# Performance work log

Measured on AMD Instinct MI355X. Metric: run time of the kernel, lower is better.

The kernel has to match this reference:

```python
import jax, jax.numpy as jnp
import numpy as np

B, S, D = 4, 2048, 1024
E = 8            # num_experts
F = 4096         # expert hidden dim (4*D)
T = B * S        # tokens
CAP = 1280       # capacity = ceil(1.25 * T / E)


def setup_inputs() -> dict:
    key = jax.random.key(0)
    k1, k2, k3, k4 = jax.random.split(key, 4)
    inputs = jax.random.normal(k1, (B, S, D), dtype=jnp.float32)
    gate_w = jax.random.normal(k2, (D, E), dtype=jnp.float32) / np.sqrt(D)
    w1 = jax.random.normal(k3, (E, D, F), dtype=jnp.float32) / np.sqrt(D)
    w2 = jax.random.normal(k4, (E, F, D), dtype=jnp.float32) / np.sqrt(F)
    return {"inputs": inputs, "gate_w": gate_w, "w1": w1, "w2": w2}


def reference(inputs, gate_w, w1, w2):
    tokens = inputs.reshape(-1, D)                       # [T, D]
    logits = tokens @ gate_w                             # [T, E] (gate, no bias)
    probs = jax.nn.softmax(logits, axis=-1)
    expert_idx = jnp.argmax(probs, axis=-1)              # top-1 routing
    mask1 = jax.nn.one_hot(expert_idx, E, dtype=tokens.dtype)        # [T, E]
    # position of each token within its chosen expert's queue
    pos = (jnp.cumsum(mask1, axis=0) - 1.0).astype(jnp.int32)        # [T, E]
    # one_hot of out-of-range (>= CAP) positions is all-zero -> capacity drop
    sec_mask = mask1[:, :, None] * jax.nn.one_hot(pos, CAP, dtype=tokens.dtype)  # [T, E, C]
    combine_weights = probs[:, :, None] * sec_mask       # [T, E, C]
    # dispatch: matmul(sec_mask.permute(1,2,0), tokens) -> [E, C, D]
    expert_input = jnp.einsum('tec,td->ecd', sec_mask, tokens)
    # grouped per-expert FFN
    h = jax.nn.relu(jnp.einsum('ecd,edf->ecf', expert_input, w1))    # [E, C, F]
    expert_output = jnp.einsum('ecf,efd->ecd', h, w2)                # [E, C, D]
    # combine: [T, E*C] @ [E*C, D]
    out = jnp.einsum('tec,ecd->td', combine_weights, expert_output)  # [T, D]
    return out.reshape(inputs.shape)
```

## Files before the change

kernel.cpp:

```cpp
#include <hip/hip_runtime.h>
#include <hip/hip_bf16.h>

#define TOKENS   8192
#define DDIM     1024
#define NEXP     8
#define FDIM     4096
#define CAPACITY 1280
#define NYT      10

typedef __attribute__((ext_vector_type(8))) __bf16 bf16x8;
typedef __attribute__((ext_vector_type(4))) __bf16 bf16x4;
typedef __attribute__((ext_vector_type(4))) float  f32x4;

typedef __attribute__((address_space(1))) const void gvoid_t;
typedef __attribute__((address_space(3))) void       lvoid_t;

__device__ __forceinline__ void async16(const void* g, void* l) {
  __builtin_amdgcn_global_load_lds((gvoid_t*)g, (lvoid_t*)l, 16, 0, 0);
}

__global__ void gate_kernel(const float* __restrict__ x, const float* __restrict__ gw,
                            int* __restrict__ eidx, float* __restrict__ prob) {
  const int t = blockIdx.x;
  const int lane = threadIdx.x;
  const float* xp = x + (size_t)t * DDIM;
  float acc[NEXP];
#pragma unroll
  for (int e = 0; e < NEXP; ++e) acc[e] = 0.f;
#pragma unroll 4
  for (int i = 0; i < DDIM / 64; ++i) {
    const int d = i * 64 + lane;
    const float xv = xp[d];
    const f32x4 g0 = *(const f32x4*)(gw + d * NEXP);
    const f32x4 g1 = *(const f32x4*)(gw + d * NEXP + 4);
    acc[0] += xv * g0[0]; acc[1] += xv * g0[1];
    acc[2] += xv * g0[2]; acc[3] += xv * g0[3];
    acc[4] += xv * g1[0]; acc[5] += xv * g1[1];
    acc[6] += xv * g1[2]; acc[7] += xv * g1[3];
  }
#pragma unroll
  for (int e = 0; e < NEXP; ++e) {
    float v = acc[e];
#pragma unroll
    for (int off = 32; off; off >>= 1) v += __shfl_xor(v, off);
    acc[e] = v;
  }
  if (lane == 0) {
    float m = acc[0]; int mi = 0;
#pragma unroll
    for (int e = 1; e < NEXP; ++e) if (acc[e] > m) { m = acc[e]; mi = e; }
    float s = 0.f;
#pragma unroll
    for (int e = 0; e < NEXP; ++e) s += __expf(acc[e] - m);
    eidx[t] = mi;
    prob[t] = 1.f / s;
  }
}

__global__ void scan_kernel(const int* __restrict__ eidx, int* __restrict__ src,
                            int* __restrict__ counts) {
  __shared__ int buf[2][NEXP][256];
  const int tid = threadIdx.x;
  for (int i = tid; i < NEXP * CAPACITY; i += 256) src[i] = -1;
  const int t0 = tid * (TOKENS / 256);
#pragma unroll
  for (int e = 0; e < NEXP; ++e) buf[0][e][tid] = 0;
  for (int k = 0; k < TOKENS / 256; ++k) {
    const int e = eidx[t0 + k];
    buf[0][e][tid]++;
  }
  __syncthreads();
  int cur = 0;
  for (int off = 1; off < 256; off <<= 1) {
#pragma unroll
    for (int e = 0; e < NEXP; ++e) {
      int v = buf[cur][e][tid];
      if (tid >= off) v += buf[cur][e][tid - off];
      buf[cur ^ 1][e][tid] = v;
    }
    __syncthreads();
    cur ^= 1;
  }
  if (tid < NEXP) counts[tid] = buf[cur][tid][255];
#pragma unroll
  for (int e = 0; e < NEXP; ++e)
    buf[cur ^ 1][e][tid] = (tid > 0) ? buf[cur][e][tid - 1] : 0;
  for (int k = 0; k < TOKENS / 256; ++k) {
    const int t = t0 + k;
    const int e = eidx[t];
    const int p = buf[cur ^ 1][e][tid]++;
    if (p < CAPACITY) src[e * CAPACITY + p] = t;
  }
}

__global__ void dispatch_kernel(const float* __restrict__ tokens, const int* __restrict__ src,
                                __bf16* __restrict__ Xb) {
  const int slot = blockIdx.x;
  const int tid  = threadIdx.x;
  const int t = src[slot];
  bf16x4* dst = (bf16x4*)(Xb + (size_t)slot * DDIM);
  bf16x4 o;
  if (t >= 0) {
    const f32x4 v = ((const f32x4*)(tokens + (size_t)t * DDIM))[tid];
    o[0] = (__bf16)v[0]; o[1] = (__bf16)v[1]; o[2] = (__bf16)v[2]; o[3] = (__bf16)v[3];
  } else {
    o[0] = (__bf16)0.f; o[1] = (__bf16)0.f; o[2] = (__bf16)0.f; o[3] = (__bf16)0.f;
  }
  dst[tid] = o;
}

__global__ void transpose_convert_kernel(const float* __restrict__ w, __bf16* __restrict__ wt,
                                         int R, int C) {
  __shared__ __bf16 tile[64][66];
  const int e = blockIdx.z;
  const float* wp = w + (size_t)e * R * C;
  __bf16* op = wt + (size_t)e * R * C;
  const int c0 = blockIdx.x * 64, r0 = blockIdx.y * 64;
  const int tid = threadIdx.x;
#pragma unroll
  for (int p = 0; p < 4; ++p) {
    const int r = p * 16 + (tid >> 4);
    const int c = (tid & 15) * 4;
    const f32x4 v = *(const f32x4*)(wp + (size_t)(r0 + r) * C + c0 + c);
    tile[r][c]     = (__bf16)v[0]; tile[r][c + 1] = (__bf16)v[1];
    tile[r][c + 2] = (__bf16)v[2]; tile[r][c + 3] = (__bf16)v[3];
  }
  __syncthreads();
#pragma unroll
  for (int p = 0; p < 2; ++p) {
    const int c  = p * 32 + (tid >> 3);
    const int rg = (tid & 7) * 8;
    bf16x8 o;
#pragma unroll
    for (int i = 0; i < 8; ++i) o[i] = tile[rg + i][c];
    *(bf16x8*)(op + (size_t)(c0 + c) * R + r0 + rg) = o;
  }
}

__global__ __launch_bounds__(256, 2)
void gemm1_kernel(const __bf16* __restrict__ A, const __bf16* __restrict__ B,
                  __bf16* __restrict__ Cbf, const int* __restrict__ counts,
                  int K, size_t sA, size_t sB, size_t sC) {
  constexpr int N  = FDIM;
  constexpr int NX = N / 128;
  __shared__ __bf16 lds[2][128 * 64];

  const int nwg = NX * NYT * NEXP;
  int wg = blockIdx.x;
  wg = (wg & 7) * (nwg >> 3) + (wg >> 3);
  const int e   = wg / (NX * NYT);
  const int rem = wg - e * (NX * NYT);
  const int ty  = rem % NYT;
  const int tx  = rem / NYT;
  const int m0  = ty * 128, n0 = tx * 128;

  const int cnt   = counts[e];
  const int tiles = (cnt + 127) >> 7;
  if (ty >= ((tiles < NYT) ? tiles : NYT)) return;

  const __bf16* Ae = A + (size_t)e * sA;
  const __bf16* Be = B + (size_t)e * sB;
  const int tid = threadIdx.x;
  const int wid = tid >> 6, lane = tid & 63;
  const int wm = wid >> 1, wn = wid & 1;
  const int rl = lane & 15, gl = lane >> 4;

  f32x4 acc[4][4];
#pragma unroll
  for (int m = 0; m < 4; ++m)
#pragma unroll
    for (int n = 0; n < 4; ++n) acc[m][n] = (f32x4){0.f, 0.f, 0.f, 0.f};

  for (int kt = 0; kt < K; kt += 64) {
#pragma unroll
    for (int i = 0; i < 4; ++i) {
      const int s   = (wid * 4 + i) * 64 + lane;
      const int row = s >> 3;
      const int cg  = (s & 7) ^ (row & 7);
      async16(Ae + (size_t)(m0 + row) * K + kt + cg * 8, &lds[0][(wid * 4 + i) * 512]);
      async16(Be + (size_t)(n0 + row) * K + kt + cg * 8, &lds[1][(wid * 4 + i) * 512]);
    }
    __syncthreads();
    const char* la = (const char*)&lds[0][0];
    const char* lb = (const char*)&lds[1][0];
#pragma unroll
    for (int kk = 0; kk < 2; ++kk) {
      bf16x8 af[4], bv[4];
#pragma unroll
      for (int m = 0; m < 4; ++m) {
        const int rowin = wm * 64 + m * 16 + rl;
        af[m] = *(const bf16x8*)(la + rowin * 128 + (((kk * 4 + gl) ^ (rowin & 7)) * 16));
      }
#pragma unroll
      for (int n = 0; n < 4; ++n) {
        const int rowin = wn * 64 + n * 16 + rl;
        bv[n] = *(const bf16x8*)(lb + rowin * 128 + (((kk * 4 + gl) ^ (rowin & 7)) * 16));
      }
#pragma unroll
      for (int m = 0; m < 4; ++m)
#pragma unroll
        for (int n = 0; n < 4; ++n)
          acc[m][n] = __builtin_amdgcn_mfma_f32_16x16x32_bf16(af[m], bv[n], acc[m][n], 0, 0, 0);
    }
    __syncthreads();
  }

  __bf16* Ce = Cbf + (size_t)e * sC;
#pragma unroll
  for (int m = 0; m < 4; ++m)
#pragma unroll
    for (int j = 0; j < 4; ++j) {
      const int row = m0 + wm * 64 + m * 16 + gl * 4 + j;
#pragma unroll
      for (int n = 0; n < 4; ++n) {
        const int col = n0 + wn * 64 + n * 16 + rl;
        float v = acc[m][n][j];
        v = v > 0.f ? v : 0.f;
        Ce[(size_t)row * N + col] = (__bf16)v;
      }
    }
}

__global__ __launch_bounds__(256, 2)
void gemm2_kernel(const __bf16* __restrict__ A, const float* __restrict__ Bw,
                  float* __restrict__ out, const int* __restrict__ src,
                  const float* __restrict__ prob, const int* __restrict__ counts,
                  int K, size_t sA, size_t sBw) {
  constexpr int N  = DDIM;
  constexpr int NX = N / 128;
  __shared__ __bf16 lds[2][128 * 64];

  const int nwg = NX * NYT * NEXP;
  int wg = blockIdx.x;
  wg = (wg & 7) * (nwg >> 3) + (wg >> 3);
  const int e   = wg / (NX * NYT);
  const int rem = wg - e * (NX * NYT);
  const int ty  = rem % NYT;
  const int tx  = rem / NYT;
  const int m0  = ty * 128, n0 = tx * 128;

  const int cnt   = counts[e];
  const int tiles = (cnt + 127) >> 7;
  if (ty >= ((tiles < NYT) ? tiles : NYT)) return;

  const __bf16* Ae = A + (size_t)e * sA;
  const float*  Be = Bw + (size_t)e * sBw;
  const int tid = threadIdx.x;
  const int wid = tid >> 6, lane = tid & 63;
  const int wm = wid >> 1, wn = wid & 1;
  const int rl = lane & 15, gl = lane >> 4;
  const int nq = tid & 31;
  const int kb = tid >> 5;

  f32x4 acc[4][4];
#pragma unroll
  for (int m = 0; m < 4; ++m)
#pragma unroll
    for (int n = 0; n < 4; ++n) acc[m][n] = (f32x4){0.f, 0.f, 0.f, 0.f};

  for (int kt = 0; kt < K; kt += 64) {
    f32x4 r[8];
#pragma unroll
    for (int i = 0; i < 8; ++i)
      r[i] = *(const f32x4*)(Be + (size_t)(kt + kb * 8 + i) * N + n0 + nq * 4);
#pragma unroll
    for (int i = 0; i < 4; ++i) {
      const int s   = (wid * 4 + i) * 64 + lane;
      const int row = s >> 3;
      const int cg  = (s & 7) ^ (row & 7);
      async16(Ae + (size_t)(m0 + row) * K + kt + cg * 8, &lds[0][(wid * 4 + i) * 512]);
    }
#pragma unroll
    for (int i2 = 0; i2 < 4; ++i2) {
      const int n  = nq * 4 + i2;
      const int sl = kb ^ (n & 7) ^ ((n >> 3) & 7);
      bf16x8 o;
#pragma unroll
      for (int i = 0; i < 8; ++i) o[i] = (__bf16)r[i][i2];
      *(bf16x8*)((char*)&lds[1][0] + n * 128 + sl * 16) = o;
    }
    __syncthreads();
    const char* la = (const char*)&lds[0][0];
    const char* lb = (const char*)&lds[1][0];
#pragma unroll
    for (int kk = 0; kk < 2; ++kk) {
      bf16x8 af[4], bv[4];
#pragma unroll
      for (int m = 0; m < 4; ++m) {
        const int rowin = wm * 64 + m * 16 + rl;
        af[m] = *(const bf16x8*)(la + rowin * 128 + (((kk * 4 + gl) ^ (rowin & 7)) * 16));
      }
#pragma unroll
      for (int n = 0; n < 4; ++n) {
        const int rowin = wn * 64 + n * 16 + rl;
        const int sl = (kk * 4 + gl) ^ (rowin & 7) ^ ((rowin >> 3) & 7);
        bv[n] = *(const bf16x8*)(lb + rowin * 128 + sl * 16);
      }
#pragma unroll
      for (int m = 0; m < 4; ++m)
#pragma unroll
        for (int n = 0; n < 4; ++n)
          acc[m][n] = __builtin_amdgcn_mfma_f32_16x16x32_bf16(af[m], bv[n], acc[m][n], 0, 0, 0);
    }
    __syncthreads();
  }

#pragma unroll
  for (int m = 0; m < 4; ++m)
#pragma unroll
    for (int j = 0; j < 4; ++j) {
      const int slot = m0 + wm * 64 + m * 16 + gl * 4 + j;
      const int t = src[e * CAPACITY + slot];
      if (t >= 0) {
        const float p = prob[t];
        float* op = out + (size_t)t * N;
#pragma unroll
        for (int n = 0; n < 4; ++n) {
          const int col = n0 + wn * 64 + n * 16 + rl;
          op[col] = p * acc[m][n][j];
        }
      }
    }
}

extern "C" void kernel_launch(void* const* d_in, const int* in_sizes, int n_in,
                              void* d_out, int out_size, void* d_ws, size_t ws_size,
                              hipStream_t stream) {
  const float* x  = (const float*)d_in[0];
  const float* gw = (const float*)d_in[1];
  const float* w1 = (const float*)d_in[2];
  const float* w2 = (const float*)d_in[3];
  float* out = (float*)d_out;

  char* ws = (char*)d_ws;
  size_t off = 0;
  auto alloc = [&](size_t bytes) {
    void* p = ws + off;
    off += (bytes + 255) & ~(size_t)255;
    return p;
  };
  __bf16* W1bT = (__bf16*)alloc((size_t)NEXP * FDIM * DDIM * 2);
  __bf16* Xb   = (__bf16*)alloc((size_t)NEXP * CAPACITY * DDIM * 2);
  __bf16* Hb   = (__bf16*)alloc((size_t)NEXP * CAPACITY * FDIM * 2);
  int*   eidx  = (int*)alloc(TOKENS * sizeof(int));
  float* prob  = (float*)alloc(TOKENS * sizeof(float));
  int*   srcm  = (int*)alloc(NEXP * CAPACITY * sizeof(int));
  int*   cnts  = (int*)alloc(NEXP * sizeof(int));
  (void)ws_size; (void)in_sizes; (void)n_in;

  hipMemsetAsync(d_out, 0, (size_t)out_size * sizeof(float), stream);

  gate_kernel<<<TOKENS, 64, 0, stream>>>(x, gw, eidx, prob);
  scan_kernel<<<1, 256, 0, stream>>>(eidx, srcm, cnts);
  dispatch_kernel<<<NEXP * CAPACITY, 256, 0, stream>>>(x, srcm, Xb);
  transpose_convert_kernel<<<dim3(FDIM / 64, DDIM / 64, NEXP), 256, 0, stream>>>(
      w1, W1bT, DDIM, FDIM);
  gemm1_kernel<<<(FDIM / 128) * NYT * NEXP, 256, 0, stream>>>(
      Xb, W1bT, Hb, cnts,
      DDIM, (size_t)CAPACITY * DDIM, (size_t)FDIM * DDIM, (size_t)CAPACITY * FDIM);
  gemm2_kernel<<<(DDIM / 128) * NYT * NEXP, 256, 0, stream>>>(
      Hb, w2, out, srcm, prob, cnts,
      FDIM, (size_t)CAPACITY * FDIM, (size_t)FDIM * DDIM);
}
```

Before: 305.0 us.

## Double-buffer LDS in gemm1 to overlap global loads with MFMA compute

Changes the first expert GEMM from a single-buffered load-sync-compute loop to a two-stage ping-pong LDS pipeline. The tile for k-step t+2 is prefetched into the buffer just consumed, with explicit vmcnt waits and scheduling barriers, so the async global-to-LDS copies overlap the MFMA work on the other buffer. This doubles LDS use per block to 64KB, which may limit the two blocks per CU requested by the launch bounds, and it relies on hand-tuned wait counts being correct.

```diff
diff --git a/kernel.cpp b/kernel.cpp
--- a/kernel.cpp
+++ b/kernel.cpp
@@ -143,7 +143,7 @@
                   int K, size_t sA, size_t sB, size_t sC) {
   constexpr int N  = FDIM;
   constexpr int NX = N / 128;
-  __shared__ __bf16 lds[2][128 * 64];
+  __shared__ __bf16 lds[2][2][128 * 64];
 
   const int nwg = NX * NYT * NEXP;
   int wg = blockIdx.x;
@@ -171,38 +171,65 @@
 #pragma unroll
     for (int n = 0; n < 4; ++n) acc[m][n] = (f32x4){0.f, 0.f, 0.f, 0.f};
 
-  for (int kt = 0; kt < K; kt += 64) {
+  auto stage = [&](int c, int kt) {
+    const int k0 = kt * 64;
 #pragma unroll
     for (int i = 0; i < 4; ++i) {
       const int s   = (wid * 4 + i) * 64 + lane;
       const int row = s >> 3;
       const int cg  = (s & 7) ^ (row & 7);
-      async16(Ae + (size_t)(m0 + row) * K + kt + cg * 8, &lds[0][(wid * 4 + i) * 512]);
-      async16(Be + (size_t)(n0 + row) * K + kt + cg * 8, &lds[1][(wid * 4 + i) * 512]);
-    }
-    __syncthreads();
-    const char* la = (const char*)&lds[0][0];
-    const char* lb = (const char*)&lds[1][0];
-#pragma unroll
-    for (int kk = 0; kk < 2; ++kk) {
-      bf16x8 af[4], bv[4];
-#pragma unroll
-      for (int m = 0; m < 4; ++m) {
-        const int rowin = wm * 64 + m * 16 + rl;
-        af[m] = *(const bf16x8*)(la + rowin * 128 + (((kk * 4 + gl) ^ (rowin & 7)) * 16));
-      }
-#pragma unroll
-      for (int n = 0; n < 4; ++n) {
-        const int rowin = wn * 64 + n * 16 + rl;
-        bv[n] = *(const bf16x8*)(lb + rowin * 128 + (((kk * 4 + gl) ^ (rowin & 7)) * 16));
-      }
-#pragma unroll
-      for (int m = 0; m < 4; ++m)
-#pragma unroll
-        for (int n = 0; n < 4; ++n)
-          acc[m][n] = __builtin_amdgcn_mfma_f32_16x16x32_bf16(af[m], bv[n], acc[m][n], 0, 0, 0);
-    }
-    __syncthreads();
+      async16(Ae + (size_t)(m0 + row) * K + k0 + cg * 8, &lds[c][0][(wid * 4 + i) * 512]);
+      async16(Be + (size_t)(n0 + row) * K + k0 + cg * 8, &lds[c][1][(wid * 4 + i) * 512]);
+    }
+  };
+
+  auto phase = [&](int c, int kk) {
+    const char* la = (const char*)&lds[c][0][0];
+    const char* lb = (const char*)&lds[c][1][0];
+    bf16x8 af[4], bv[4];
+#pragma unroll
+    for (int m = 0; m < 4; ++m) {
+      const int rowin = wm * 64 + m * 16 + rl;
+      af[m] = *(const bf16x8*)(la + rowin * 128 + (((kk * 4 + gl) ^ (rowin & 7)) * 16));
+    }
+#pragma unroll
+    for (int n = 0; n < 4; ++n) {
+      const int rowin = wn * 64 + n * 16 + rl;
+      bv[n] = *(const bf16x8*)(lb + rowin * 128 + (((kk * 4 + gl) ^ (rowin & 7)) * 16));
+    }
+#pragma unroll
+    for (int m = 0; m < 4; ++m)
+#pragma unroll
+      for (int n = 0; n < 4; ++n)
+        acc[m][n] = __builtin_amdgcn_mfma_f32_16x16x32_bf16(af[m], bv[n], acc[m][n], 0, 0, 0);
+  };
+
+  const int nkt = K >> 6;
+  stage(0, 0);
+  stage(1, 1);
+  asm volatile("s_waitcnt vmcnt(8)" ::: "memory");
+  __builtin_amdgcn_sched_barrier(0);
+  __builtin_amdgcn_s_barrier();
+  __builtin_amdgcn_sched_barrier(0);
+
+  for (int t = 0; t < nkt; ++t) {
+    const int c = t & 1;
+    phase(c, 0);
+    phase(c, 1);
+    if (t + 1 < nkt) {
+      __builtin_amdgcn_sched_barrier(0);
+      __builtin_amdgcn_s_barrier();
+      __builtin_amdgcn_sched_barrier(0);
+      if (t + 2 < nkt) {
+        stage(c, t + 2);
+        asm volatile("s_waitcnt vmcnt(8)" ::: "memory");
+      } else {
+        asm volatile("s_waitcnt vmcnt(0)" ::: "memory");
+      }
+      __builtin_amdgcn_sched_barrier(0);
+      __builtin_amdgcn_s_barrier();
+      __builtin_amdgcn_sched_barrier(0);
+    }
   }
 
   __bf16* Ce = Cbf + (size_t)e * sC;
```

After: 305.0 us. About the same (-0.0%).

## Restructure gemm1 into 256x256 tiles with double-buffered async LDS pipeline

Applied to the files above, without the earlier changes.

Rewrites the first expert GEMM to use 256x256 output tiles computed by 512-thread workgroups. Global-to-LDS loads for the next K-step run into a second LDS buffer, staged in pieces between MFMA phases, with explicit vmcnt waits, scheduling barriers and setprio around MFMA bursts. The intent is to hide load latency behind compute and raise data reuse per LDS tile. In exchange it uses more LDS (128 KB) and more accumulator registers, and the larger tiles waste more work on partially filled experts.

```diff
diff --git a/kernel.cpp b/kernel.cpp
--- a/kernel.cpp
+++ b/kernel.cpp
@@ -7,6 +7,7 @@
 #define FDIM     4096
 #define CAPACITY 1280
 #define NYT      10
+#define NYT1     5
 
 typedef __attribute__((ext_vector_type(8))) __bf16 bf16x8;
 typedef __attribute__((ext_vector_type(4))) __bf16 bf16x4;
@@ -18,6 +19,9 @@
 __device__ __forceinline__ void async16(const void* g, void* l) {
   __builtin_amdgcn_global_load_lds((gvoid_t*)g, (lvoid_t*)l, 16, 0, 0);
 }
+
+#define SBAR do { __builtin_amdgcn_sched_barrier(0); __builtin_amdgcn_s_barrier(); \
+                  __builtin_amdgcn_sched_barrier(0); } while (0)
 
 __global__ void gate_kernel(const float* __restrict__ x, const float* __restrict__ gw,
                             int* __restrict__ eidx, float* __restrict__ prob) {
@@ -137,84 +141,142 @@
   }
 }
 
-__global__ __launch_bounds__(256, 2)
+__global__ __launch_bounds__(512, 2)
 void gemm1_kernel(const __bf16* __restrict__ A, const __bf16* __restrict__ B,
                   __bf16* __restrict__ Cbf, const int* __restrict__ counts,
                   int K, size_t sA, size_t sB, size_t sC) {
   constexpr int N  = FDIM;
-  constexpr int NX = N / 128;
-  __shared__ __bf16 lds[2][128 * 64];
-
-  const int nwg = NX * NYT * NEXP;
+  constexpr int NX = N / 256;
+  __shared__ __bf16 lds[2][2][2][128 * 64];
+
+  const int nwg = NX * NYT1 * NEXP;
   int wg = blockIdx.x;
   wg = (wg & 7) * (nwg >> 3) + (wg >> 3);
-  const int e   = wg / (NX * NYT);
-  const int rem = wg - e * (NX * NYT);
-  const int ty  = rem % NYT;
-  const int tx  = rem / NYT;
-  const int m0  = ty * 128, n0 = tx * 128;
+  const int e   = wg / (NX * NYT1);
+  const int rem = wg - e * (NX * NYT1);
+  const int ty  = rem % NYT1;
+  const int tx  = rem / NYT1;
+  const int m0  = ty * 256, n0 = tx * 256;
 
   const int cnt   = counts[e];
-  const int tiles = (cnt + 127) >> 7;
-  if (ty >= ((tiles < NYT) ? tiles : NYT)) return;
+  const int tiles = (cnt + 255) >> 8;
+  if (ty >= ((tiles < NYT1) ? tiles : NYT1)) return;
 
   const __bf16* Ae = A + (size_t)e * sA;
   const __bf16* Be = B + (size_t)e * sB;
   const int tid = threadIdx.x;
   const int wid = tid >> 6, lane = tid & 63;
-  const int wm = wid >> 1, wn = wid & 1;
+  const int wm = wid >> 2, wn = wid & 3;
   const int rl = lane & 15, gl = lane >> 4;
 
-  f32x4 acc[4][4];
-#pragma unroll
-  for (int m = 0; m < 4; ++m)
+  f32x4 acc[8][4];
+#pragma unroll
+  for (int m = 0; m < 8; ++m)
 #pragma unroll
     for (int n = 0; n < 4; ++n) acc[m][n] = (f32x4){0.f, 0.f, 0.f, 0.f};
 
-  for (int kt = 0; kt < K; kt += 64) {
-#pragma unroll
-    for (int i = 0; i < 4; ++i) {
-      const int s   = (wid * 4 + i) * 64 + lane;
-      const int row = s >> 3;
-      const int cg  = (s & 7) ^ (row & 7);
-      async16(Ae + (size_t)(m0 + row) * K + kt + cg * 8, &lds[0][(wid * 4 + i) * 512]);
-      async16(Be + (size_t)(n0 + row) * K + kt + cg * 8, &lds[1][(wid * 4 + i) * 512]);
-    }
-    __syncthreads();
-    const char* la = (const char*)&lds[0][0];
-    const char* lb = (const char*)&lds[1][0];
-#pragma unroll
-    for (int kk = 0; kk < 2; ++kk) {
-      bf16x8 af[4], bv[4];
-#pragma unroll
-      for (int m = 0; m < 4; ++m) {
-        const int rowin = wm * 64 + m * 16 + rl;
-        af[m] = *(const bf16x8*)(la + rowin * 128 + (((kk * 4 + gl) ^ (rowin & 7)) * 16));
-      }
-#pragma unroll
-      for (int n = 0; n < 4; ++n) {
-        const int rowin = wn * 64 + n * 16 + rl;
-        bv[n] = *(const bf16x8*)(lb + rowin * 128 + (((kk * 4 + gl) ^ (rowin & 7)) * 16));
-      }
-#pragma unroll
-      for (int m = 0; m < 4; ++m)
-#pragma unroll
-        for (int n = 0; n < 4; ++n)
-          acc[m][n] = __builtin_amdgcn_mfma_f32_16x16x32_bf16(af[m], bv[n], acc[m][n], 0, 0, 0);
-    }
-    __syncthreads();
+  auto stageA = [&](int c, int half, int kt) {
+    const __bf16* base = Ae + (size_t)(m0 + half * 128) * K + kt * 64;
+#pragma unroll
+    for (int i = 0; i < 2; ++i) {
+      const int chunk = i * 8 + wid;
+      const int s = chunk * 64 + lane;
+      const int row = s >> 3, cg = (s & 7) ^ (row & 7);
+      async16(base + (size_t)row * K + cg * 8, (char*)&lds[c][0][half][0] + chunk * 1024);
+    }
+  };
+  auto stageB = [&](int c, int half, int kt) {
+    const __bf16* base = Be + (size_t)(n0 + half * 128) * K + kt * 64;
+#pragma unroll
+    for (int i = 0; i < 2; ++i) {
+      const int chunk = i * 8 + wid;
+      const int s = chunk * 64 + lane;
+      const int row = s >> 3, cg = (s & 7) ^ (row & 7);
+      async16(base + (size_t)row * K + cg * 8, (char*)&lds[c][1][half][0] + chunk * 1024);
+    }
+  };
+  auto rdA = [&](int c, int mf, int kk) -> bf16x8 {
+    const int row = mf * 16 + rl;
+    const int g = (kk * 4 + gl) ^ (row & 7);
+    return *(const bf16x8*)((const char*)&lds[c][0][wm][0] + row * 128 + g * 16);
+  };
+  auto rdB = [&](int c, int nf, int kk) -> bf16x8 {
+    const int rb = wn * 64 + nf * 16 + rl;
+    const int half = rb >> 7, row = rb & 127;
+    const int g = (kk * 4 + gl) ^ (row & 7);
+    return *(const bf16x8*)((const char*)&lds[c][1][half][0] + row * 128 + g * 16);
+  };
+
+  const int nkt = K >> 6;
+  stageA(0, 0, 0); stageA(0, 1, 0); stageB(0, 0, 0); stageB(0, 1, 0);
+  stageA(1, 0, 1); stageA(1, 1, 1);
+  asm volatile("s_waitcnt vmcnt(4)" ::: "memory");
+  SBAR;
+
+  for (int u = 0; u < nkt; ++u) {
+    const int c = u & 1;
+    bf16x8 a0[8], a1[8], b0[4], b1[4];
+#pragma unroll
+    for (int mf = 0; mf < 8; ++mf) a0[mf] = rdA(c, mf, 0);
+#pragma unroll
+    for (int nf = 0; nf < 4; ++nf) b0[nf] = rdB(c, nf, 0);
+    if (u + 1 < nkt) stageB(c ^ 1, 0, u + 1);
+    SBAR;
+    __builtin_amdgcn_s_setprio(1);
+#pragma unroll
+    for (int mf = 0; mf < 4; ++mf)
+#pragma unroll
+      for (int nf = 0; nf < 4; ++nf)
+        acc[mf][nf] = __builtin_amdgcn_mfma_f32_16x16x32_bf16(a0[mf], b0[nf], acc[mf][nf], 0, 0, 0);
+    __builtin_amdgcn_s_setprio(0);
+#pragma unroll
+    for (int mf = 0; mf < 8; ++mf) a1[mf] = rdA(c, mf, 1);
+#pragma unroll
+    for (int nf = 0; nf < 4; ++nf) b1[nf] = rdB(c, nf, 1);
+    if (u + 1 < nkt) stageB(c ^ 1, 1, u + 1);
+    SBAR;
+    __builtin_amdgcn_s_setprio(1);
+#pragma unroll
+    for (int mf = 4; mf < 8; ++mf)
+#pragma unroll
+      for (int nf = 0; nf < 4; ++nf)
+        acc[mf][nf] = __builtin_amdgcn_mfma_f32_16x16x32_bf16(a0[mf], b0[nf], acc[mf][nf], 0, 0, 0);
+    __builtin_amdgcn_s_setprio(0);
+    if (u + 2 < nkt) stageA(c, 0, u + 2);
+    SBAR;
+    __builtin_amdgcn_s_setprio(1);
+#pragma unroll
+    for (int mf = 0; mf < 4; ++mf)
+#pragma unroll
+      for (int nf = 0; nf < 4; ++nf)
+        acc[mf][nf] = __builtin_amdgcn_mfma_f32_16x16x32_bf16(a1[mf], b1[nf], acc[mf][nf], 0, 0, 0);
+    __builtin_amdgcn_s_setprio(0);
+    if (u + 2 < nkt) {
+      stageA(c, 1, u + 2);
+      asm volatile("s_waitcnt vmcnt(4)" ::: "memory");
+    } else {
+      asm volatile("s_waitcnt vmcnt(0)" ::: "memory");
+    }
+    SBAR;
+    __builtin_amdgcn_s_setprio(1);
+#pragma unroll
+    for (int mf = 4; mf < 8; ++mf)
+#pragma unroll
+      for (int nf = 0; nf < 4; ++nf)
+        acc[mf][nf] = __builtin_amdgcn_mfma_f32_16x16x32_bf16(a1[mf], b1[nf], acc[mf][nf], 0, 0, 0);
+    __builtin_amdgcn_s_setprio(0);
   }
 
   __bf16* Ce = Cbf + (size_t)e * sC;
 #pragma unroll
-  for (int m = 0; m < 4; ++m)
+  for (int mf = 0; mf < 8; ++mf)
 #pragma unroll
     for (int j = 0; j < 4; ++j) {
-      const int row = m0 + wm * 64 + m * 16 + gl * 4 + j;
-#pragma unroll
-      for (int n = 0; n < 4; ++n) {
-        const int col = n0 + wn * 64 + n * 16 + rl;
-        float v = acc[m][n][j];
+      const int row = m0 + wm * 128 + mf * 16 + gl * 4 + j;
+#pragma unroll
+      for (int nf = 0; nf < 4; ++nf) {
+        const int col = n0 + wn * 64 + nf * 16 + rl;
+        float v = acc[mf][nf][j];
         v = v > 0.f ? v : 0.f;
         Ce[(size_t)row * N + col] = (__bf16)v;
       }
@@ -355,7 +417,7 @@
   dispatch_kernel<<<NEXP * CAPACITY, 256, 0, stream>>>(x, srcm, Xb);
   transpose_convert_kernel<<<dim3(FDIM / 64, DDIM / 64, NEXP), 256, 0, stream>>>(
       w1, W1bT, DDIM, FDIM);
-  gemm1_kernel<<<(FDIM / 128) * NYT * NEXP, 256, 0, stream>>>(
+  gemm1_kernel<<<(FDIM / 256) * NYT1 * NEXP, 512, 0, stream>>>(
       Xb, W1bT, Hb, cnts,
       DDIM, (size_t)CAPACITY * DDIM, (size_t)FDIM * DDIM, (size_t)CAPACITY * FDIM);
   gemm2_kernel<<<(DDIM / 128) * NYT * NEXP, 256, 0, stream>>>(
```

Result: no change. 309.5 us (+1.5%).

## Split gemm2 along K into two halves and reduce partials in a separate kernel

Applied to the files above, without the earlier changes.

The second expert GEMM now launches twice as many workgroups, each covering half of the K=4096 reduction, and writes unscaled fp32 partial tiles into a new workspace buffer. A new reduce kernel sums the two partials per capacity slot, applies the routing probability and scatters the row to the output token. The aim is more parallelism and better CU occupancy for gemm2 (640 tiles before). The cost is an extra ~84 MB of fp32 partial writes and reads plus another kernel launch.

```diff
diff --git a/kernel.cpp b/kernel.cpp
--- a/kernel.cpp
+++ b/kernel.cpp
@@ -223,18 +223,19 @@
 
 __global__ __launch_bounds__(256, 2)
 void gemm2_kernel(const __bf16* __restrict__ A, const float* __restrict__ Bw,
-                  float* __restrict__ out, const int* __restrict__ src,
-                  const float* __restrict__ prob, const int* __restrict__ counts,
+                  float* __restrict__ P, const int* __restrict__ counts,
                   int K, size_t sA, size_t sBw) {
   constexpr int N  = DDIM;
   constexpr int NX = N / 128;
   __shared__ __bf16 lds[2][128 * 64];
 
-  const int nwg = NX * NYT * NEXP;
+  const int nwg = 2 * NX * NYT * NEXP;
   int wg = blockIdx.x;
   wg = (wg & 7) * (nwg >> 3) + (wg >> 3);
-  const int e   = wg / (NX * NYT);
-  const int rem = wg - e * (NX * NYT);
+  const int half = wg / (NX * NYT * NEXP);
+  int base = wg - half * (NX * NYT * NEXP);
+  const int e   = base / (NX * NYT);
+  const int rem = base - e * (NX * NYT);
   const int ty  = rem % NYT;
   const int tx  = rem / NYT;
   const int m0  = ty * 128, n0 = tx * 128;
@@ -258,7 +259,9 @@
 #pragma unroll
     for (int n = 0; n < 4; ++n) acc[m][n] = (f32x4){0.f, 0.f, 0.f, 0.f};
 
-  for (int kt = 0; kt < K; kt += 64) {
+  const int k0 = half * (K >> 1);
+  const int k1 = k0 + (K >> 1);
+  for (int kt = k0; kt < k1; kt += 64) {
     f32x4 r[8];
 #pragma unroll
     for (int i = 0; i < 8; ++i)
@@ -305,22 +308,34 @@
     __syncthreads();
   }
 
+  float* Pe = P + ((size_t)half * NEXP * CAPACITY + (size_t)e * CAPACITY) * DDIM;
 #pragma unroll
   for (int m = 0; m < 4; ++m)
 #pragma unroll
     for (int j = 0; j < 4; ++j) {
       const int slot = m0 + wm * 64 + m * 16 + gl * 4 + j;
-      const int t = src[e * CAPACITY + slot];
-      if (t >= 0) {
-        const float p = prob[t];
-        float* op = out + (size_t)t * N;
-#pragma unroll
-        for (int n = 0; n < 4; ++n) {
-          const int col = n0 + wn * 64 + n * 16 + rl;
-          op[col] = p * acc[m][n][j];
-        }
-      }
-    }
+      float* op = Pe + (size_t)slot * DDIM;
+#pragma unroll
+      for (int n = 0; n < 4; ++n) {
+        const int col = n0 + wn * 64 + n * 16 + rl;
+        op[col] = acc[m][n][j];
+      }
+    }
+}
+
+__global__ void reduce_kernel(const float* __restrict__ P, const int* __restrict__ src,
+                              const float* __restrict__ prob, float* __restrict__ out) {
+  const int slot = blockIdx.x;
+  const int t = src[slot];
+  if (t < 0) return;
+  const int tid = threadIdx.x;
+  const float p = prob[t];
+  const f32x4 a = ((const f32x4*)(P + (size_t)slot * DDIM))[tid];
+  const f32x4 b = ((const f32x4*)(P + ((size_t)NEXP * CAPACITY + slot) * DDIM))[tid];
+  f32x4 o;
+  o[0] = p * (a[0] + b[0]); o[1] = p * (a[1] + b[1]);
+  o[2] = p * (a[2] + b[2]); o[3] = p * (a[3] + b[3]);
+  ((f32x4*)(out + (size_t)t * DDIM))[tid] = o;
 }
 
 extern "C" void kernel_launch(void* const* d_in, const int* in_sizes, int n_in,
@@ -342,6 +357,7 @@
   __bf16* W1bT = (__bf16*)alloc((size_t)NEXP * FDIM * DDIM * 2);
   __bf16* Xb   = (__bf16*)alloc((size_t)NEXP * CAPACITY * DDIM * 2);
   __bf16* Hb   = (__bf16*)alloc((size_t)NEXP * CAPACITY * FDIM * 2);
+  float* Pbuf  = (float*)alloc((size_t)2 * NEXP * CAPACITY * DDIM * 4);
   int*   eidx  = (int*)alloc(TOKENS * sizeof(int));
   float* prob  = (float*)alloc(TOKENS * sizeof(float));
   int*   srcm  = (int*)alloc(NEXP * CAPACITY * sizeof(int));
@@ -358,7 +374,8 @@
   gemm1_kernel<<<(FDIM / 128) * NYT * NEXP, 256, 0, stream>>>(
       Xb, W1bT, Hb, cnts,
       DDIM, (size_t)CAPACITY * DDIM, (size_t)FDIM * DDIM, (size_t)CAPACITY * FDIM);
-  gemm2_kernel<<<(DDIM / 128) * NYT * NEXP, 256, 0, stream>>>(
-      Hb, w2, out, srcm, prob, cnts,
+  gemm2_kernel<<<2 * (DDIM / 128) * NYT * NEXP, 256, 0, stream>>>(
+      Hb, w2, Pbuf, cnts,
       FDIM, (size_t)CAPACITY * FDIM, (size_t)FDIM * DDIM);
-}
+  reduce_kernel<<<NEXP * CAPACITY, 256, 0, stream>>>(Pbuf, srcm, prob, out);
+}
```

Result: slower. 375.7 us (+23.2%).
